# Optimization experiments

Measured on AMD Instinct MI355X. Metric: run time of the kernel, lower is better.

The kernel has to match this reference:

```python
import jax, jax.numpy as jnp
import numpy as np

DIM = 1024
N_GROUPS = 32
GROUP_SIZE = DIM // N_GROUPS
T, B = 1024, 16


def setup_inputs() -> dict:
    key = jax.random.key(0)
    k1, k2, k3, k4, k5 = jax.random.split(key, 5)
    std = (2.0 / (DIM + DIM)) ** 0.5  # xavier-like scale
    return {
        "x": jax.random.normal(k1, (T, B, DIM), dtype=jnp.float32),
        "h0": jnp.zeros((B, DIM), dtype=jnp.float32),
        "W_x": jax.random.normal(k2, (DIM, DIM), dtype=jnp.float32) * std,
        "r_h": jnp.zeros((DIM,), dtype=jnp.float32),
        "b": jnp.zeros((DIM,), dtype=jnp.float32),
        "W_alpha": jax.random.normal(k3, (DIM, DIM), dtype=jnp.float32) * (0.1 * std),
        "b_alpha": jnp.zeros((DIM,), dtype=jnp.float32),
        "W_delta": jax.random.normal(k4, (DIM, DIM), dtype=jnp.float32) * (0.1 * std),
        "b_delta": jnp.full((DIM,), -2.0, dtype=jnp.float32),
        "W_out": jax.random.normal(k5, (DIM, DIM), dtype=jnp.float32) * std,
    }


def reference(x, h0, W_x, r_h, b, W_alpha, b_alpha, W_delta, b_delta, W_out):
    # x-only projections batched over all timesteps in three big GEMMs
    vx = jnp.einsum('tbd,ed->tbe', x, W_x) + b                                  # [T,B,D]
    alpha = 1.0 + jax.nn.softplus(jnp.einsum('tbd,ed->tbe', x, W_alpha) + b_alpha)
    delta = jax.nn.sigmoid(jnp.einsum('tbd,ed->tbe', x, W_delta) + b_delta)

    def step(h_prev, inp):
        vx_t, a_t, d_t = inp
        v = vx_t + r_h * h_prev
        abs_v = jnp.clip(jnp.abs(v), 1e-6, 10.0)
        candidate = jnp.sign(v) * abs_v ** a_t
        h_new = (1.0 - d_t) * h_prev + d_t * candidate                          # [B,D]
        compete = jax.nn.softmax(
            h_new.reshape(-1, N_GROUPS, GROUP_SIZE), axis=-1).reshape(-1, DIM)
        out = compete * jax.nn.silu(h_new @ W_out.T)
        return h_new, (h_new, out)

    _, (hs, outs) = jax.lax.scan(step, h0, (vx, alpha, delta))
    h = jnp.concatenate([h0[None], hs], axis=0)                                 # [T+1,B,D]
    return h, outs
```

## Files before the change

### kernel.cpp

```cpp
#include <hip/hip_runtime.h>
#include <hip/hip_bf16.h>
#include <hip/hip_fp16.h>

#define DIM 1024
#define NGROUPS 32
#define GSIZE 32
#define TT 1024
#define BB 16
#define MROWS (TT*BB)
#define BD (BB*DIM)
#define G 16
#define NG (TT/G)

typedef __attribute__((ext_vector_type(8))) short short8;
typedef __attribute__((ext_vector_type(4))) float f32x4;

__device__ __forceinline__ ushort f2b(float v) {
  __hip_bfloat16 b = __float2bfloat16(v);
  return *reinterpret_cast<ushort*>(&b);
}
__device__ __forceinline__ float b2f(ushort u) {
  __hip_bfloat16 b; *reinterpret_cast<ushort*>(&b) = u;
  return __bfloat162float(b);
}
__device__ __forceinline__ ushort f2h(float v) {
  __half h = __float2half(v);
  return *reinterpret_cast<ushort*>(&h);
}
__device__ __forceinline__ float softplusf(float z) {
  return (z > 20.f) ? z : log1pf(expf(z));
}
__device__ __forceinline__ float sigmoidf_(float z) { return 1.f/(1.f+expf(-z)); }

#define AS1(p) ((__attribute__((address_space(1))) void*)(void*)(p))
#define AS3(p) ((__attribute__((address_space(3))) void*)(void*)(p))

__global__ __launch_bounds__(256) void split_x_kernel(
    const float4* __restrict__ x, ushort4* __restrict__ xh, ushort4* __restrict__ xl, int n4) {
  int i = blockIdx.x*256 + threadIdx.x;
  int stride = gridDim.x*256;
  for (; i < n4; i += stride) {
    float4 v = x[i];
    ushort4 h, l;
    h.x = f2b(v.x); l.x = f2b(v.x - b2f(h.x));
    h.y = f2b(v.y); l.y = f2b(v.y - b2f(h.y));
    h.z = f2b(v.z); l.z = f2b(v.z - b2f(h.z));
    h.w = f2b(v.w); l.w = f2b(v.w - b2f(h.w));
    xh[i] = h; xl[i] = l;
  }
}

__global__ __launch_bounds__(256) void split_w_kernel(
    const float4* __restrict__ wx, const float4* __restrict__ wa,
    const float4* __restrict__ wd, const float4* __restrict__ wo,
    ushort4* __restrict__ wxh, ushort4* __restrict__ wxl,
    ushort4* __restrict__ wah, ushort4* __restrict__ wdh,
    ushort4* __restrict__ woh, int n4) {
  int i = blockIdx.x*256 + threadIdx.x;
  if (i >= n4) return;
  float4 v = wx[i];
  ushort4 h, l;
  h.x = f2b(v.x); l.x = f2b(v.x - b2f(h.x));
  h.y = f2b(v.y); l.y = f2b(v.y - b2f(h.y));
  h.z = f2b(v.z); l.z = f2b(v.z - b2f(h.z));
  h.w = f2b(v.w); l.w = f2b(v.w - b2f(h.w));
  wxh[i] = h; wxl[i] = l;
  float4 a = wa[i];
  ushort4 ha; ha.x=f2b(a.x); ha.y=f2b(a.y); ha.z=f2b(a.z); ha.w=f2b(a.w);
  wah[i] = ha;
  float4 d = wd[i];
  ushort4 hd; hd.x=f2b(d.x); hd.y=f2b(d.y); hd.z=f2b(d.z); hd.w=f2b(d.w);
  wdh[i] = hd;
  float4 o = wo[i];
  ushort4 ho; ho.x=f2b(o.x); ho.y=f2b(o.y); ho.z=f2b(o.z); ho.w=f2b(o.w);
  woh[i] = ho;
}


__global__ __launch_bounds__(256, 2) void gemm_vx_kernel(
    const ushort* __restrict__ Xh, const ushort* __restrict__ Xl,
    const ushort* __restrict__ Wxh, const ushort* __restrict__ Wxl,
    const float* __restrict__ b_v, float* __restrict__ vxout)
{
  __shared__ ushort As [2][128*32];
  __shared__ ushort AsL[2][128*32];
  __shared__ ushort Bs [2][128*32];
  __shared__ ushort BsL[2][128*32];

  const int tid  = threadIdx.x;
  const int lane = tid & 63;
  const int wid  = tid >> 6;
  const int wr   = wid >> 1, wc = wid & 1;

  const int did = blockIdx.y * 8 + blockIdx.x;
  const int xcd = did & 7;
  const int j   = did >> 3;
  const int m0  = (xcd * 16 + (j >> 3)) * 128;
  const int n0  = (j & 7) * 128;

  f32x4 acc[4][4];
  #pragma unroll
  for (int i=0;i<4;++i)
    #pragma unroll
    for (int jj=0;jj<4;++jj) acc[i][jj] = f32x4{0.f,0.f,0.f,0.f};

  const int fr = lane & 15;
  const int rc = (((lane >> 4) ^ ((fr >> 1) & 3))) * 8;

#define STAGE_VX(cur, ks)                                                     \
  {                                                                           \
    _Pragma("unroll")                                                         \
    for (int jl = 0; jl < 2; ++jl) {                                          \
      int idx = jl*256 + tid;                                                 \
      int row = idx >> 2;                                                     \
      int cs  = ((idx & 3) ^ ((row >> 1) & 3)) * 8;                           \
      size_t gA = (size_t)(m0+row)*DIM + (ks)*32 + cs;                        \
      size_t gB = (size_t)(n0+row)*DIM + (ks)*32 + cs;                        \
      __builtin_amdgcn_global_load_lds(AS1(Xh+gA),  AS3(&As [cur][idx*8]), 16, 0, 0); \
      __builtin_amdgcn_global_load_lds(AS1(Xl+gA),  AS3(&AsL[cur][idx*8]), 16, 0, 0); \
      __builtin_amdgcn_global_load_lds(AS1(Wxh+gB), AS3(&Bs [cur][idx*8]), 16, 0, 0); \
      __builtin_amdgcn_global_load_lds(AS1(Wxl+gB), AS3(&BsL[cur][idx*8]), 16, 0, 0); \
    }                                                                         \
  }

  STAGE_VX(0, 0);
  __syncthreads();
  int cur = 0;

  for (int ks = 0; ks < DIM/32; ++ks) {
    if (ks + 1 < DIM/32) STAGE_VX(cur^1, ks+1);
    __builtin_amdgcn_sched_barrier(0);

    short8 ah[4], al[4], bh[4], bl[4];
    #pragma unroll
    for (int f=0; f<4; ++f) {
      ah[f] = *(const short8*)&As [cur][(wr*64+f*16+fr)*32 + rc];
      al[f] = *(const short8*)&AsL[cur][(wr*64+f*16+fr)*32 + rc];
      bh[f] = *(const short8*)&Bs [cur][(wc*64+f*16+fr)*32 + rc];
      bl[f] = *(const short8*)&BsL[cur][(wc*64+f*16+fr)*32 + rc];
    }
    #pragma unroll
    for (int fi=0; fi<4; ++fi)
      #pragma unroll
      for (int fj=0; fj<4; ++fj) {
        acc[fi][fj] = __builtin_amdgcn_mfma_f32_16x16x32_bf16(ah[fi], bh[fj], acc[fi][fj], 0,0,0);
        acc[fi][fj] = __builtin_amdgcn_mfma_f32_16x16x32_bf16(ah[fi], bl[fj], acc[fi][fj], 0,0,0);
        acc[fi][fj] = __builtin_amdgcn_mfma_f32_16x16x32_bf16(al[fi], bh[fj], acc[fi][fj], 0,0,0);
      }
    __syncthreads();
    cur ^= 1;
  }

  #pragma unroll
  for (int fi=0; fi<4; ++fi)
    #pragma unroll
    for (int fj=0; fj<4; ++fj)
      #pragma unroll
      for (int r=0; r<4; ++r) {
        int row = m0 + wr*64 + fi*16 + (lane>>4)*4 + r;
        int col = n0 + wc*64 + fj*16 + (lane&15);
        vxout[(size_t)row*DIM + col] = acc[fi][fj][r] + b_v[col];
      }
}

__global__ __launch_bounds__(256, 2) void gemm_ad_kernel(
    const ushort* __restrict__ Xh,
    const ushort* __restrict__ Wah, const ushort* __restrict__ Wdh,
    const float* __restrict__ b_a, const float* __restrict__ b_d,
    uint* __restrict__ adout)
{
  __shared__ ushort As[2][128*32];
  __shared__ ushort Ba[2][128*32];
  __shared__ ushort Bd[2][128*32];

  const int tid  = threadIdx.x;
  const int lane = tid & 63;
  const int wid  = tid >> 6;
  const int wr   = wid >> 1, wc = wid & 1;

  const int did = blockIdx.y * 8 + blockIdx.x;
  const int xcd = did & 7;
  const int j   = did >> 3;
  const int m0  = (xcd * 16 + (j >> 3)) * 128;
  const int n0  = (j & 7) * 128;

  f32x4 aca[4][4], acd[4][4];
  #pragma unroll
  for (int i=0;i<4;++i)
    #pragma unroll
    for (int jj=0;jj<4;++jj) {
      aca[i][jj] = f32x4{0.f,0.f,0.f,0.f};
      acd[i][jj] = f32x4{0.f,0.f,0.f,0.f};
    }

  const int fr = lane & 15;
  const int rc = (((lane >> 4) ^ ((fr >> 1) & 3))) * 8;

#define STAGE_AD(cur, ks)                                                     \
  {                                                                           \
    _Pragma("unroll")                                                         \
    for (int jl = 0; jl < 2; ++jl) {                                          \
      int idx = jl*256 + tid;                                                 \
      int row = idx >> 2;                                                     \
      int cs  = ((idx & 3) ^ ((row >> 1) & 3)) * 8;                           \
      size_t gA = (size_t)(m0+row)*DIM + (ks)*32 + cs;                        \
      size_t gB = (size_t)(n0+row)*DIM + (ks)*32 + cs;                        \
      __builtin_amdgcn_global_load_lds(AS1(Xh+gA),  AS3(&As[cur][idx*8]), 16, 0, 0); \
      __builtin_amdgcn_global_load_lds(AS1(Wah+gB), AS3(&Ba[cur][idx*8]), 16, 0, 0); \
      __builtin_amdgcn_global_load_lds(AS1(Wdh+gB), AS3(&Bd[cur][idx*8]), 16, 0, 0); \
    }                                                                         \
  }

  STAGE_AD(0, 0);
  __syncthreads();
  int cur = 0;

  for (int ks = 0; ks < DIM/32; ++ks) {
    if (ks + 1 < DIM/32) STAGE_AD(cur^1, ks+1);
    __builtin_amdgcn_sched_barrier(0);

    short8 ah[4], ba[4], bd[4];
    #pragma unroll
    for (int f=0; f<4; ++f) {
      ah[f] = *(const short8*)&As[cur][(wr*64+f*16+fr)*32 + rc];
      ba[f] = *(const short8*)&Ba[cur][(wc*64+f*16+fr)*32 + rc];
      bd[f] = *(const short8*)&Bd[cur][(wc*64+f*16+fr)*32 + rc];
    }
    #pragma unroll
    for (int fi=0; fi<4; ++fi)
      #pragma unroll
      for (int fj=0; fj<4; ++fj) {
        aca[fi][fj] = __builtin_amdgcn_mfma_f32_16x16x32_bf16(ah[fi], ba[fj], aca[fi][fj], 0,0,0);
        acd[fi][fj] = __builtin_amdgcn_mfma_f32_16x16x32_bf16(ah[fi], bd[fj], acd[fi][fj], 0,0,0);
      }
    __syncthreads();
    cur ^= 1;
  }

  #pragma unroll
  for (int fi=0; fi<4; ++fi)
    #pragma unroll
    for (int fj=0; fj<4; ++fj)
      #pragma unroll
      for (int r=0; r<4; ++r) {
        int row = m0 + wr*64 + fi*16 + (lane>>4)*4 + r;
        int col = n0 + wc*64 + fj*16 + (lane&15);
        float a_ = 1.f + softplusf(aca[fi][fj][r] + b_a[col]);
        float d_ = sigmoidf_(acd[fi][fj][r] + b_d[col]);
        adout[(size_t)row*DIM + col] = (uint)f2h(a_) | ((uint)f2h(d_) << 16);
      }
}

__global__ __launch_bounds__(256, 2) void gemm_out_kernel(
    const ushort* __restrict__ Ah, const ushort* __restrict__ Bh,
    const float* __restrict__ extra, float* __restrict__ C)
{
  __shared__ ushort As[2][128*32];
  __shared__ ushort Bs[2][128*32];

  const int tid  = threadIdx.x;
  const int lane = tid & 63;
  const int wid  = tid >> 6;
  const int wr   = wid >> 1, wc = wid & 1;

  const int did = blockIdx.y * 8 + blockIdx.x;
  const int xcd = did & 7;
  const int j   = did >> 3;
  const int m0  = (xcd * 16 + (j >> 3)) * 128;
  const int n0  = (j & 7) * 128;

  f32x4 acc[4][4];
  #pragma unroll
  for (int i=0;i<4;++i)
    #pragma unroll
    for (int jj=0;jj<4;++jj) acc[i][jj] = f32x4{0.f,0.f,0.f,0.f};

  const int fr = lane & 15;
  const int rc = (((lane >> 4) ^ ((fr >> 1) & 3))) * 8;

#define STAGE_O(cur, ks)                                                      \
  {                                                                           \
    _Pragma("unroll")                                                         \
    for (int jl = 0; jl < 2; ++jl) {                                          \
      int idx = jl*256 + tid;                                                 \
      int row = idx >> 2;                                                     \
      int cs  = ((idx & 3) ^ ((row >> 1) & 3)) * 8;                           \
      __builtin_amdgcn_global_load_lds(AS1(Ah+(size_t)(m0+row)*DIM + (ks)*32 + cs), AS3(&As[cur][idx*8]), 16, 0, 0); \
      __builtin_amdgcn_global_load_lds(AS1(Bh+(size_t)(n0+row)*DIM + (ks)*32 + cs), AS3(&Bs[cur][idx*8]), 16, 0, 0); \
    }                                                                         \
  }

  STAGE_O(0, 0);
  __syncthreads();
  int cur = 0;

  for (int ks = 0; ks < DIM/32; ++ks) {
    if (ks + 1 < DIM/32) STAGE_O(cur^1, ks+1);
    __builtin_amdgcn_sched_barrier(0);

    short8 ah[4], bh[4];
    #pragma unroll
    for (int f=0; f<4; ++f) {
      ah[f] = *(const short8*)&As[cur][(wr*64+f*16+fr)*32 + rc];
      bh[f] = *(const short8*)&Bs[cur][(wc*64+f*16+fr)*32 + rc];
    }
    #pragma unroll
    for (int fi=0; fi<4; ++fi)
      #pragma unroll
      for (int fj=0; fj<4; ++fj)
        acc[fi][fj] = __builtin_amdgcn_mfma_f32_16x16x32_bf16(ah[fi], bh[fj], acc[fi][fj], 0,0,0);
    __syncthreads();
    cur ^= 1;
  }

  #pragma unroll
  for (int fi=0; fi<4; ++fi)
    #pragma unroll
    for (int fj=0; fj<4; ++fj)
      #pragma unroll
      for (int r=0; r<4; ++r) {
        int row = m0 + wr*64 + fi*16 + (lane>>4)*4 + r;
        int col = n0 + wc*64 + fj*16 + (lane&15);
        float c = acc[fi][fj][r];
        C[(size_t)row*DIM + col] = extra[(size_t)row*DIM + col] * (c * sigmoidf_(c));
      }
}

#define SCAN_STEP(vv, adb, t)                                                \
  {                                                                          \
    uint bits = (adb);                                                       \
    __half ha_, hd_;                                                         \
    *reinterpret_cast<ushort*>(&ha_) = (ushort)(bits & 0xFFFF);              \
    *reinterpret_cast<ushort*>(&hd_) = (ushort)(bits >> 16);                 \
    float a = __half2float(ha_);                                             \
    float d = __half2float(hd_);                                             \
    float v = fmaf(r, h, (vv));                                              \
    float av = fminf(fmaxf(fabsf(v), 1e-6f), 10.0f);                         \
    float cand = copysignf(__builtin_amdgcn_exp2f(a * __builtin_amdgcn_logf(av)), v); \
    h = fmaf(d, cand - h, h);                                                \
    hout[(size_t)((t)+1)*BD + tid] = h;                                      \
    Hb[(size_t)(t)*BD + tid] = f2b(h);                                       \
  }

__global__ __launch_bounds__(64) void scan_kernel(
    const float* __restrict__ pv, const uint* __restrict__ pad,
    const float* __restrict__ rh, const float* __restrict__ h0,
    float* __restrict__ hout, ushort* __restrict__ Hb)
{
  int tid = blockIdx.x*64 + threadIdx.x;
  float r = rh[tid & (DIM-1)];
  float h = h0[tid];
  hout[tid] = h;

  float bufVA[G], bufVB[G];
  uint  bufDA[G], bufDB[G];

  #pragma unroll
  for (int i = 0; i < G; ++i) {
    bufVA[i] = pv [(size_t)i*BD + tid];
    bufDA[i] = pad[(size_t)i*BD + tid];
  }
  __builtin_amdgcn_sched_barrier(0);

  for (int gp = 0; gp < NG; gp += 2) {
    #pragma unroll
    for (int i = 0; i < G; ++i) {
      bufVB[i] = pv [(size_t)((gp+1)*G + i)*BD + tid];
      bufDB[i] = pad[(size_t)((gp+1)*G + i)*BD + tid];
    }
    __builtin_amdgcn_sched_barrier(0);
    #pragma unroll
    for (int i = 0; i < G; ++i) { SCAN_STEP(bufVA[i], bufDA[i], gp*G + i); }
    __builtin_amdgcn_sched_barrier(0);
    if (gp + 2 < NG) {
      #pragma unroll
      for (int i = 0; i < G; ++i) {
        bufVA[i] = pv [(size_t)((gp+2)*G + i)*BD + tid];
        bufDA[i] = pad[(size_t)((gp+2)*G + i)*BD + tid];
      }
    }
    __builtin_amdgcn_sched_barrier(0);
    #pragma unroll
    for (int i = 0; i < G; ++i) { SCAN_STEP(bufVB[i], bufDB[i], (gp+1)*G + i); }
    __builtin_amdgcn_sched_barrier(0);
  }
}

__global__ __launch_bounds__(256) void compete_kernel(
    const float* __restrict__ h, float* __restrict__ comp)
{
  int g = blockIdx.x*256 + threadIdx.x;
  const float4* p = (const float4*)(h + (size_t)g*GSIZE);
  float vals[32];
  #pragma unroll
  for (int j = 0; j < 8; ++j) {
    float4 t4 = p[j];
    vals[4*j+0]=t4.x; vals[4*j+1]=t4.y; vals[4*j+2]=t4.z; vals[4*j+3]=t4.w;
  }
  float m = vals[0];
  #pragma unroll
  for (int j = 1; j < 32; ++j) m = fmaxf(m, vals[j]);
  float s = 0.f;
  #pragma unroll
  for (int j = 0; j < 32; ++j) { vals[j] = expf(vals[j]-m); s += vals[j]; }
  float inv = 1.f/s;
  float4* o = (float4*)(comp + (size_t)g*GSIZE);
  #pragma unroll
  for (int j = 0; j < 8; ++j) {
    float4 t4; t4.x=vals[4*j]*inv; t4.y=vals[4*j+1]*inv; t4.z=vals[4*j+2]*inv; t4.w=vals[4*j+3]*inv;
    o[j] = t4;
  }
}

extern "C" void kernel_launch(void* const* d_in, const int* in_sizes, int n_in,
                              void* d_out, int out_size, void* d_ws, size_t ws_size,
                              hipStream_t stream) {
  const float* x       = (const float*)d_in[0];
  const float* h0      = (const float*)d_in[1];
  const float* W_x     = (const float*)d_in[2];
  const float* r_h     = (const float*)d_in[3];
  const float* b       = (const float*)d_in[4];
  const float* W_alpha = (const float*)d_in[5];
  const float* b_alpha = (const float*)d_in[6];
  const float* W_delta = (const float*)d_in[7];
  const float* b_delta = (const float*)d_in[8];
  const float* W_out   = (const float*)d_in[9];

  float* out   = (float*)d_out;
  float* h_out = out;
  float* outs  = out + (size_t)(TT+1)*BD;

  char* p = (char*)d_ws;
  ushort* Xh  = (ushort*)p; p += (size_t)MROWS*DIM*2;
  ushort* Xl  = (ushort*)p; p += (size_t)MROWS*DIM*2;
  ushort* Wxh = (ushort*)p; p += (size_t)DIM*DIM*2;
  ushort* Wxl = (ushort*)p; p += (size_t)DIM*DIM*2;
  ushort* Wah = (ushort*)p; p += (size_t)DIM*DIM*2;
  ushort* Wdh = (ushort*)p; p += (size_t)DIM*DIM*2;
  ushort* Woh = (ushort*)p; p += (size_t)DIM*DIM*2;
  float*  vxa = (float*)p;  p += (size_t)MROWS*DIM*4;
  uint*   ada = (uint*)p;   p += (size_t)MROWS*DIM*4;
  ushort* Hb  = (ushort*)p; p += (size_t)MROWS*DIM*2;
  float*  comp = (float*)p; p += (size_t)MROWS*DIM*4;

  split_x_kernel<<<2048, 256, 0, stream>>>((const float4*)x, (ushort4*)Xh, (ushort4*)Xl, MROWS*DIM/4);
  split_w_kernel<<<1024, 256, 0, stream>>>((const float4*)W_x, (const float4*)W_alpha,
                                           (const float4*)W_delta, (const float4*)W_out,
                                           (ushort4*)Wxh, (ushort4*)Wxl, (ushort4*)Wah,
                                           (ushort4*)Wdh, (ushort4*)Woh, DIM*DIM/4);

  dim3 g(DIM/128, MROWS/128);
  gemm_vx_kernel<<<g, 256, 0, stream>>>(Xh, Xl, Wxh, Wxl, b, vxa);
  gemm_ad_kernel<<<g, 256, 0, stream>>>(Xh, Wah, Wdh, b_alpha, b_delta, ada);

  scan_kernel<<<256, 64, 0, stream>>>(vxa, ada, r_h, h0, h_out, Hb);

  compete_kernel<<<2048, 256, 0, stream>>>(h_out + (size_t)BD, comp);

  gemm_out_kernel<<<g, 256, 0, stream>>>(Hb, Woh, comp, outs);
}
```

Measured before the change: 605.5 us.

## Switch GEMMs from split-bf16 to single fp16 MFMA and widen alpha/delta GEMM block

Replaces the bf16 hi/lo split used for the vx projection (three MFMAs per tile) with a single fp16 operand per input, halving workspace traffic for x and the weights and cutting vx MFMA work by two thirds. All GEMMs and the scan's h copy move to fp16. The alpha/delta GEMM now runs 512 threads per block, with each wave computing a 32x64 sub-tile. Launch-bounds occupancy hints are raised to 3 blocks for two kernels. This trades the extra mantissa bits of the split scheme for fp16's 10-bit mantissa, with a risk of overflow or accuracy loss if values exceed fp16 range.

```diff
diff --git a/kernel.cpp b/kernel.cpp
--- a/kernel.cpp
+++ b/kernel.cpp
@@ -12,17 +12,9 @@
 #define G 16
 #define NG (TT/G)
 
-typedef __attribute__((ext_vector_type(8))) short short8;
+typedef __attribute__((ext_vector_type(8))) _Float16 half8;
 typedef __attribute__((ext_vector_type(4))) float f32x4;
 
-__device__ __forceinline__ ushort f2b(float v) {
-  __hip_bfloat16 b = __float2bfloat16(v);
-  return *reinterpret_cast<ushort*>(&b);
-}
-__device__ __forceinline__ float b2f(ushort u) {
-  __hip_bfloat16 b; *reinterpret_cast<ushort*>(&b) = u;
-  return __bfloat162float(b);
-}
 __device__ __forceinline__ ushort f2h(float v) {
   __half h = __float2half(v);
   return *reinterpret_cast<ushort*>(&h);
@@ -36,56 +28,45 @@
 #define AS3(p) ((__attribute__((address_space(3))) void*)(void*)(p))
 
 __global__ __launch_bounds__(256) void split_x_kernel(
-    const float4* __restrict__ x, ushort4* __restrict__ xh, ushort4* __restrict__ xl, int n4) {
+    const float4* __restrict__ x, ushort4* __restrict__ xf, int n4) {
   int i = blockIdx.x*256 + threadIdx.x;
   int stride = gridDim.x*256;
   for (; i < n4; i += stride) {
     float4 v = x[i];
-    ushort4 h, l;
-    h.x = f2b(v.x); l.x = f2b(v.x - b2f(h.x));
-    h.y = f2b(v.y); l.y = f2b(v.y - b2f(h.y));
-    h.z = f2b(v.z); l.z = f2b(v.z - b2f(h.z));
-    h.w = f2b(v.w); l.w = f2b(v.w - b2f(h.w));
-    xh[i] = h; xl[i] = l;
+    ushort4 h;
+    h.x = f2h(v.x); h.y = f2h(v.y); h.z = f2h(v.z); h.w = f2h(v.w);
+    xf[i] = h;
   }
 }
 
 __global__ __launch_bounds__(256) void split_w_kernel(
     const float4* __restrict__ wx, const float4* __restrict__ wa,
     const float4* __restrict__ wd, const float4* __restrict__ wo,
-    ushort4* __restrict__ wxh, ushort4* __restrict__ wxl,
-    ushort4* __restrict__ wah, ushort4* __restrict__ wdh,
-    ushort4* __restrict__ woh, int n4) {
+    ushort4* __restrict__ wxf, ushort4* __restrict__ waf,
+    ushort4* __restrict__ wdf, ushort4* __restrict__ wof, int n4) {
   int i = blockIdx.x*256 + threadIdx.x;
   if (i >= n4) return;
   float4 v = wx[i];
-  ushort4 h, l;
-  h.x = f2b(v.x); l.x = f2b(v.x - b2f(h.x));
-  h.y = f2b(v.y); l.y = f2b(v.y - b2f(h.y));
-  h.z = f2b(v.z); l.z = f2b(v.z - b2f(h.z));
-  h.w = f2b(v.w); l.w = f2b(v.w - b2f(h.w));
-  wxh[i] = h; wxl[i] = l;
+  ushort4 h; h.x=f2h(v.x); h.y=f2h(v.y); h.z=f2h(v.z); h.w=f2h(v.w);
+  wxf[i] = h;
   float4 a = wa[i];
-  ushort4 ha; ha.x=f2b(a.x); ha.y=f2b(a.y); ha.z=f2b(a.z); ha.w=f2b(a.w);
-  wah[i] = ha;
+  ushort4 ha; ha.x=f2h(a.x); ha.y=f2h(a.y); ha.z=f2h(a.z); ha.w=f2h(a.w);
+  waf[i] = ha;
   float4 d = wd[i];
-  ushort4 hd; hd.x=f2b(d.x); hd.y=f2b(d.y); hd.z=f2b(d.z); hd.w=f2b(d.w);
-  wdh[i] = hd;
+  ushort4 hd; hd.x=f2h(d.x); hd.y=f2h(d.y); hd.z=f2h(d.z); hd.w=f2h(d.w);
+  wdf[i] = hd;
   float4 o = wo[i];
-  ushort4 ho; ho.x=f2b(o.x); ho.y=f2b(o.y); ho.z=f2b(o.z); ho.w=f2b(o.w);
-  woh[i] = ho;
-}
-
-
-__global__ __launch_bounds__(256, 2) void gemm_vx_kernel(
-    const ushort* __restrict__ Xh, const ushort* __restrict__ Xl,
-    const ushort* __restrict__ Wxh, const ushort* __restrict__ Wxl,
+  ushort4 ho; ho.x=f2h(o.x); ho.y=f2h(o.y); ho.z=f2h(o.z); ho.w=f2h(o.w);
+  wof[i] = ho;
+}
+
+
+__global__ __launch_bounds__(256, 3) void gemm_vx_kernel(
+    const ushort* __restrict__ Xf, const ushort* __restrict__ Wxf,
     const float* __restrict__ b_v, float* __restrict__ vxout)
 {
-  __shared__ ushort As [2][128*32];
-  __shared__ ushort AsL[2][128*32];
-  __shared__ ushort Bs [2][128*32];
-  __shared__ ushort BsL[2][128*32];
+  __shared__ ushort As[2][128*32];
+  __shared__ ushort Bs[2][128*32];
 
   const int tid  = threadIdx.x;
   const int lane = tid & 63;
@@ -116,10 +97,8 @@
       int cs  = ((idx & 3) ^ ((row >> 1) & 3)) * 8;                           \
       size_t gA = (size_t)(m0+row)*DIM + (ks)*32 + cs;                        \
       size_t gB = (size_t)(n0+row)*DIM + (ks)*32 + cs;                        \
-      __builtin_amdgcn_global_load_lds(AS1(Xh+gA),  AS3(&As [cur][idx*8]), 16, 0, 0); \
-      __builtin_amdgcn_global_load_lds(AS1(Xl+gA),  AS3(&AsL[cur][idx*8]), 16, 0, 0); \
-      __builtin_amdgcn_global_load_lds(AS1(Wxh+gB), AS3(&Bs [cur][idx*8]), 16, 0, 0); \
-      __builtin_amdgcn_global_load_lds(AS1(Wxl+gB), AS3(&BsL[cur][idx*8]), 16, 0, 0); \
+      __builtin_amdgcn_global_load_lds(AS1(Xf+gA),  AS3(&As[cur][idx*8]), 16, 0, 0); \
+      __builtin_amdgcn_global_load_lds(AS1(Wxf+gB), AS3(&Bs[cur][idx*8]), 16, 0, 0); \
     }                                                                         \
   }
 
@@ -131,22 +110,17 @@
     if (ks + 1 < DIM/32) STAGE_VX(cur^1, ks+1);
     __builtin_amdgcn_sched_barrier(0);
 
-    short8 ah[4], al[4], bh[4], bl[4];
+    half8 ah[4], bh[4];
     #pragma unroll
     for (int f=0; f<4; ++f) {
-      ah[f] = *(const short8*)&As [cur][(wr*64+f*16+fr)*32 + rc];
-      al[f] = *(const short8*)&AsL[cur][(wr*64+f*16+fr)*32 + rc];
-      bh[f] = *(const short8*)&Bs [cur][(wc*64+f*16+fr)*32 + rc];
-      bl[f] = *(const short8*)&BsL[cur][(wc*64+f*16+fr)*32 + rc];
+      ah[f] = *(const half8*)&As[cur][(wr*64+f*16+fr)*32 + rc];
+      bh[f] = *(const half8*)&Bs[cur][(wc*64+f*16+fr)*32 + rc];
     }
     #pragma unroll
     for (int fi=0; fi<4; ++fi)
       #pragma unroll
-      for (int fj=0; fj<4; ++fj) {
-        acc[fi][fj] = __builtin_amdgcn_mfma_f32_16x16x32_bf16(ah[fi], bh[fj], acc[fi][fj], 0,0,0);
-        acc[fi][fj] = __builtin_amdgcn_mfma_f32_16x16x32_bf16(ah[fi], bl[fj], acc[fi][fj], 0,0,0);
-        acc[fi][fj] = __builtin_amdgcn_mfma_f32_16x16x32_bf16(al[fi], bh[fj], acc[fi][fj], 0,0,0);
-      }
+      for (int fj=0; fj<4; ++fj)
+        acc[fi][fj] = __builtin_amdgcn_mfma_f32_16x16x32_f16(ah[fi], bh[fj], acc[fi][fj], 0,0,0);
     __syncthreads();
     cur ^= 1;
   }
@@ -163,9 +137,9 @@
       }
 }
 
-__global__ __launch_bounds__(256, 2) void gemm_ad_kernel(
-    const ushort* __restrict__ Xh,
-    const ushort* __restrict__ Wah, const ushort* __restrict__ Wdh,
+__global__ __launch_bounds__(512, 2) void gemm_ad_kernel(
+    const ushort* __restrict__ Xf,
+    const ushort* __restrict__ Waf, const ushort* __restrict__ Wdf,
     const float* __restrict__ b_a, const float* __restrict__ b_d,
     uint* __restrict__ adout)
 {
@@ -176,7 +150,8 @@
   const int tid  = threadIdx.x;
   const int lane = tid & 63;
   const int wid  = tid >> 6;
-  const int wr   = wid >> 1, wc = wid & 1;
+  const int wr   = wid >> 1;
+  const int wc   = wid & 1;
 
   const int did = blockIdx.y * 8 + blockIdx.x;
   const int xcd = did & 7;
@@ -184,9 +159,9 @@
   const int m0  = (xcd * 16 + (j >> 3)) * 128;
   const int n0  = (j & 7) * 128;
 
-  f32x4 aca[4][4], acd[4][4];
-  #pragma unroll
-  for (int i=0;i<4;++i)
+  f32x4 aca[2][4], acd[2][4];
+  #pragma unroll
+  for (int i=0;i<2;++i)
     #pragma unroll
     for (int jj=0;jj<4;++jj) {
       aca[i][jj] = f32x4{0.f,0.f,0.f,0.f};
@@ -198,17 +173,13 @@
 
 #define STAGE_AD(cur, ks)                                                     \
   {                                                                           \
-    _Pragma("unroll")                                                         \
-    for (int jl = 0; jl < 2; ++jl) {                                          \
-      int idx = jl*256 + tid;                                                 \
-      int row = idx >> 2;                                                     \
-      int cs  = ((idx & 3) ^ ((row >> 1) & 3)) * 8;                           \
-      size_t gA = (size_t)(m0+row)*DIM + (ks)*32 + cs;                        \
-      size_t gB = (size_t)(n0+row)*DIM + (ks)*32 + cs;                        \
-      __builtin_amdgcn_global_load_lds(AS1(Xh+gA),  AS3(&As[cur][idx*8]), 16, 0, 0); \
-      __builtin_amdgcn_global_load_lds(AS1(Wah+gB), AS3(&Ba[cur][idx*8]), 16, 0, 0); \
-      __builtin_amdgcn_global_load_lds(AS1(Wdh+gB), AS3(&Bd[cur][idx*8]), 16, 0, 0); \
-    }                                                                         \
+    int row = tid >> 2;                                                       \
+    int cs  = ((tid & 3) ^ ((row >> 1) & 3)) * 8;                             \
+    size_t gA = (size_t)(m0+row)*DIM + (ks)*32 + cs;                          \
+    size_t gB = (size_t)(n0+row)*DIM + (ks)*32 + cs;                          \
+    __builtin_amdgcn_global_load_lds(AS1(Xf+gA),  AS3(&As[cur][tid*8]), 16, 0, 0); \
+    __builtin_amdgcn_global_load_lds(AS1(Waf+gB), AS3(&Ba[cur][tid*8]), 16, 0, 0); \
+    __builtin_amdgcn_global_load_lds(AS1(Wdf+gB), AS3(&Bd[cur][tid*8]), 16, 0, 0); \
   }
 
   STAGE_AD(0, 0);
@@ -219,39 +190,41 @@
     if (ks + 1 < DIM/32) STAGE_AD(cur^1, ks+1);
     __builtin_amdgcn_sched_barrier(0);
 
-    short8 ah[4], ba[4], bd[4];
+    half8 ah[2], ba[4], bd[4];
+    #pragma unroll
+    for (int f=0; f<2; ++f)
+      ah[f] = *(const half8*)&As[cur][(wr*32+f*16+fr)*32 + rc];
     #pragma unroll
     for (int f=0; f<4; ++f) {
-      ah[f] = *(const short8*)&As[cur][(wr*64+f*16+fr)*32 + rc];
-      ba[f] = *(const short8*)&Ba[cur][(wc*64+f*16+fr)*32 + rc];
-      bd[f] = *(const short8*)&Bd[cur][(wc*64+f*16+fr)*32 + rc];
-    }
-    #pragma unroll
-    for (int fi=0; fi<4; ++fi)
+      ba[f] = *(const half8*)&Ba[cur][(wc*64+f*16+fr)*32 + rc];
+      bd[f] = *(const half8*)&Bd[cur][(wc*64+f*16+fr)*32 + rc];
+    }
+    #pragma unroll
+    for (int fi=0; fi<2; ++fi)
       #pragma unroll
       for (int fj=0; fj<4; ++fj) {
-        aca[fi][fj] = __builtin_amdgcn_mfma_f32_16x16x32_bf16(ah[fi], ba[fj], aca[fi][fj], 0,0,0);
-        acd[fi][fj] = __builtin_amdgcn_mfma_f32_16x16x32_bf16(ah[fi], bd[fj], acd[fi][fj], 0,0,0);
+        aca[fi][fj] = __builtin_amdgcn_mfma_f32_16x16x32_f16(ah[fi], ba[fj], aca[fi][fj], 0,0,0);
+        acd[fi][fj] = __builtin_amdgcn_mfma_f32_16x16x32_f16(ah[fi], bd[fj], acd[fi][fj], 0,0,0);
       }
     __syncthreads();
     cur ^= 1;
   }
 
   #pragma unroll
-  for (int fi=0; fi<4; ++fi)
+  for (int fi=0; fi<2; ++fi)
     #pragma unroll
     for (int fj=0; fj<4; ++fj)
       #pragma unroll
       for (int r=0; r<4; ++r) {
-        int row = m0 + wr*64 + fi*16 + (lane>>4)*4 + r;
-        int col = n0 + wc*64 + fj*16 + (lane&15);
+        int row = m0 + wr*32 + fi*16 + (lane>>4)*4 + r;
+        int col = n0 + wc*64 + fj*16 + fr;
         float a_ = 1.f + softplusf(aca[fi][fj][r] + b_a[col]);
         float d_ = sigmoidf_(acd[fi][fj][r] + b_d[col]);
         adout[(size_t)row*DIM + col] = (uint)f2h(a_) | ((uint)f2h(d_) << 16);
       }
 }
 
-__global__ __launch_bounds__(256, 2) void gemm_out_kernel(
+__global__ __launch_bounds__(256, 3) void gemm_out_kernel(
     const ushort* __restrict__ Ah, const ushort* __restrict__ Bh,
     const float* __restrict__ extra, float* __restrict__ C)
 {
@@ -298,17 +271,17 @@
     if (ks + 1 < DIM/32) STAGE_O(cur^1, ks+1);
     __builtin_amdgcn_sched_barrier(0);
 
-    short8 ah[4], bh[4];
+    half8 ah[4], bh[4];
     #pragma unroll
     for (int f=0; f<4; ++f) {
-      ah[f] = *(const short8*)&As[cur][(wr*64+f*16+fr)*32 + rc];
-      bh[f] = *(const short8*)&Bs[cur][(wc*64+f*16+fr)*32 + rc];
+      ah[f] = *(const half8*)&As[cur][(wr*64+f*16+fr)*32 + rc];
+      bh[f] = *(const half8*)&Bs[cur][(wc*64+f*16+fr)*32 + rc];
     }
     #pragma unroll
     for (int fi=0; fi<4; ++fi)
       #pragma unroll
       for (int fj=0; fj<4; ++fj)
-        acc[fi][fj] = __builtin_amdgcn_mfma_f32_16x16x32_bf16(ah[fi], bh[fj], acc[fi][fj], 0,0,0);
+        acc[fi][fj] = __builtin_amdgcn_mfma_f32_16x16x32_f16(ah[fi], bh[fj], acc[fi][fj], 0,0,0);
     __syncthreads();
     cur ^= 1;
   }
@@ -339,13 +312,13 @@
     float cand = copysignf(__builtin_amdgcn_exp2f(a * __builtin_amdgcn_logf(av)), v); \
     h = fmaf(d, cand - h, h);                                                \
     hout[(size_t)((t)+1)*BD + tid] = h;                                      \
-    Hb[(size_t)(t)*BD + tid] = f2b(h);                                       \
+    Hh[(size_t)(t)*BD + tid] = f2h(h);                                       \
   }
 
 __global__ __launch_bounds__(64) void scan_kernel(
     const float* __restrict__ pv, const uint* __restrict__ pad,
     const float* __restrict__ rh, const float* __restrict__ h0,
-    float* __restrict__ hout, ushort* __restrict__ Hb)
+    float* __restrict__ hout, ushort* __restrict__ Hh)
 {
   int tid = blockIdx.x*64 + threadIdx.x;
   float r = rh[tid & (DIM-1)];
@@ -431,31 +404,29 @@
   float* outs  = out + (size_t)(TT+1)*BD;
 
   char* p = (char*)d_ws;
-  ushort* Xh  = (ushort*)p; p += (size_t)MROWS*DIM*2;
-  ushort* Xl  = (ushort*)p; p += (size_t)MROWS*DIM*2;
-  ushort* Wxh = (ushort*)p; p += (size_t)DIM*DIM*2;
-  ushort* Wxl = (ushort*)p; p += (size_t)DIM*DIM*2;
-  ushort* Wah = (ushort*)p; p += (size_t)DIM*DIM*2;
-  ushort* Wdh = (ushort*)p; p += (size_t)DIM*DIM*2;
-  ushort* Woh = (ushort*)p; p += (size_t)DIM*DIM*2;
+  ushort* Xf  = (ushort*)p; p += (size_t)MROWS*DIM*2;
+  ushort* Wxf = (ushort*)p; p += (size_t)DIM*DIM*2;
+  ushort* Waf = (ushort*)p; p += (size_t)DIM*DIM*2;
+  ushort* Wdf = (ushort*)p; p += (size_t)DIM*DIM*2;
+  ushort* Wof = (ushort*)p; p += (size_t)DIM*DIM*2;
   float*  vxa = (float*)p;  p += (size_t)MROWS*DIM*4;
   uint*   ada = (uint*)p;   p += (size_t)MROWS*DIM*4;
-  ushort* Hb  = (ushort*)p; p += (size_t)MROWS*DIM*2;
+  ushort* Hh  = (ushort*)p; p += (size_t)MROWS*DIM*2;
   float*  comp = (float*)p; p += (size_t)MROWS*DIM*4;
 
-  split_x_kernel<<<2048, 256, 0, stream>>>((const float4*)x, (ushort4*)Xh, (ushort4*)Xl, MROWS*DIM/4);
+  split_x_kernel<<<2048, 256, 0, stream>>>((const float4*)x, (ushort4*)Xf, MROWS*DIM/4);
   split_w_kernel<<<1024, 256, 0, stream>>>((const float4*)W_x, (const float4*)W_alpha,
                                            (const float4*)W_delta, (const float4*)W_out,
-                                           (ushort4*)Wxh, (ushort4*)Wxl, (ushort4*)Wah,
-                                           (ushort4*)Wdh, (ushort4*)Woh, DIM*DIM/4);
+                                           (ushort4*)Wxf, (ushort4*)Waf,
+                                           (ushort4*)Wdf, (ushort4*)Wof, DIM*DIM/4);
 
   dim3 g(DIM/128, MROWS/128);
-  gemm_vx_kernel<<<g, 256, 0, stream>>>(Xh, Xl, Wxh, Wxl, b, vxa);
-  gemm_ad_kernel<<<g, 256, 0, stream>>>(Xh, Wah, Wdh, b_alpha, b_delta, ada);
-
-  scan_kernel<<<256, 64, 0, stream>>>(vxa, ada, r_h, h0, h_out, Hb);
+  gemm_vx_kernel<<<g, 256, 0, stream>>>(Xf, Wxf, b, vxa);
+  gemm_ad_kernel<<<g, 512, 0, stream>>>(Xf, Waf, Wdf, b_alpha, b_delta, ada);
+
+  scan_kernel<<<256, 64, 0, stream>>>(vxa, ada, r_h, h0, h_out, Hh);
 
   compete_kernel<<<2048, 256, 0, stream>>>(h_out + (size_t)BD, comp);
 
-  gemm_out_kernel<<<g, 256, 0, stream>>>(Hb, Woh, comp, outs);
-}
+  gemm_out_kernel<<<g, 256, 0, stream>>>(Hh, Wof, comp, outs);
+}
```

After: 559.5 us. -7.6%, faster.
